# Optimization experiments

Measured on AMD Instinct MI355X. Metric: run time of the kernel, lower is better.

Reference implementation:

```python
import jax, jax.numpy as jnp
import numpy as np

B, S, H, A = 64, 4096, 256, 128


def entmax15(z):
    # exact entmax-1.5 along the last axis (Peters & Martins 2019)
    z = z / 2.0
    z = z - jnp.max(z, axis=-1, keepdims=True)
    zs = -jnp.sort(-z, axis=-1)                      # descending sort
    n = zs.shape[-1]
    k = jnp.arange(1, n + 1, dtype=z.dtype)
    mean = jnp.cumsum(zs, axis=-1) / k
    mean_sq = jnp.cumsum(zs * zs, axis=-1) / k
    ss = k * (mean_sq - mean * mean)
    delta = jnp.clip((1.0 - ss) / k, 0.0)
    tau = mean - jnp.sqrt(delta)
    k_star = jnp.sum(tau <= zs, axis=-1)             # support size per row
    tau_star = jnp.take_along_axis(tau, (k_star - 1)[..., None], axis=-1)
    return jnp.square(jnp.clip(z - tau_star, 0.0))


def setup_inputs() -> dict:
    key = jax.random.key(0)
    k0, k1, k2, k3, k4 = jax.random.split(key, 5)
    lim1 = 1.0 / np.sqrt(H)
    lim2 = 1.0 / np.sqrt(A)
    return {
        "lstm_output": jax.random.normal(k0, (B, S, H), dtype=jnp.float32),
        "W1": jax.random.uniform(k1, (H, A), jnp.float32, -lim1, lim1),
        "b1": jax.random.uniform(k2, (A,), jnp.float32, -lim1, lim1),
        "W2": jax.random.uniform(k3, (A, 1), jnp.float32, -lim2, lim2),
        "b2": jax.random.uniform(k4, (1,), jnp.float32, -lim2, lim2),
    }


def reference(lstm_output, W1, b1, W2, b2):
    # score MLP: Linear -> Tanh -> Linear -> squeeze(-1)  => [B, S]
    h = jnp.tanh(jnp.einsum("bsh,ha->bsa", lstm_output, W1) + b1)
    scores = (jnp.einsum("bsa,ao->bso", h, W2) + b2)[..., 0]
    weights = entmax15(scores)                       # entmax over seq axis (dim=1)
    context = jnp.einsum("bsh,bs->bh", lstm_output, weights)
    return (context, weights)
```

## Files before the change

### kernel.cpp

```cpp
#include <hip/hip_runtime.h>
#include <hip/hip_bf16.h>

#define BB 64
#define SS 4096
#define HH 256
#define AA 128
#define MT 128
#define BK 64
#define XST 72

typedef __fp16 fp16v2 __attribute__((ext_vector_type(2)));
typedef _Float16 half4v __attribute__((ext_vector_type(4)));
typedef _Float16 half8v __attribute__((ext_vector_type(8)));
typedef float floatx16 __attribute__((ext_vector_type(16)));

__device__ __forceinline__ float fast_tanh(float x) {
    float xc = fminf(fmaxf(x, -9.0f), 9.0f);
    float e = __expf(2.0f * xc);
    return 1.0f - __fdividef(2.0f, e + 1.0f);
}

__global__ void convert_w1(const float* __restrict__ W1, _Float16* __restrict__ Wt) {
    int n = blockIdx.x;
    int k = threadIdx.x;
    Wt[n * HH + k] = (_Float16)W1[k * AA + n];
}

__global__ __launch_bounds__(256) void score_mfma(
    const float* __restrict__ X,
    const _Float16* __restrict__ Wt,
    const float* __restrict__ b1,
    const float* __restrict__ W2,
    const float* __restrict__ b2,
    float* __restrict__ scores)
{
    __shared__ float smem_f[9216];
    _Float16* Xs = (_Float16*)smem_f;
    _Float16* Ws = (_Float16*)smem_f + MT * XST;
    float* part = smem_f;

    const int tid   = threadIdx.x;
    const int m0    = blockIdx.x * MT;
    const int wid   = tid >> 6;
    const int lane  = tid & 63;
    const int lrow  = lane & 31;
    const int lhalf = lane >> 5;
    const int wr    = (wid & 1) * 64;
    const int wc    = (wid >> 1) * 64;

    floatx16 acc[2][2];
    #pragma unroll
    for (int i = 0; i < 2; ++i)
        #pragma unroll
        for (int j = 0; j < 2; ++j)
            #pragma unroll
            for (int r = 0; r < 16; ++r) acc[i][j][r] = 0.0f;

    for (int k0 = 0; k0 < HH; k0 += BK) {
        #pragma unroll
        for (int p = 0; p < 8; ++p) {
            int idx = tid + p * 256;
            int row = idx >> 4, c4 = idx & 15;
            float4 v = *(const float4*)(X + (size_t)(m0 + row) * HH + k0 + c4 * 4);
            union { fp16v2 h2[2]; half4v h4; } u;
            u.h2[0] = __builtin_amdgcn_cvt_pkrtz(v.x, v.y);
            u.h2[1] = __builtin_amdgcn_cvt_pkrtz(v.z, v.w);
            *(half4v*)(Xs + row * XST + c4 * 4) = u.h4;
        }
        #pragma unroll
        for (int p = 0; p < 4; ++p) {
            int idx = tid + p * 256;
            int n = idx >> 3, u2 = idx & 7;
            *(uint4*)(Ws + n * XST + u2 * 8) =
                *(const uint4*)(Wt + (size_t)n * HH + k0 + u2 * 8);
        }
        __syncthreads();
        #pragma unroll
        for (int kk = 0; kk < BK; kk += 16) {
            half8v a0 = *(half8v*)(Xs + (wr + lrow) * XST + kk + lhalf * 8);
            half8v a1 = *(half8v*)(Xs + (wr + 32 + lrow) * XST + kk + lhalf * 8);
            half8v b0 = *(half8v*)(Ws + (wc + lrow) * XST + kk + lhalf * 8);
            half8v bq = *(half8v*)(Ws + (wc + 32 + lrow) * XST + kk + lhalf * 8);
            acc[0][0] = __builtin_amdgcn_mfma_f32_32x32x16_f16(a0, b0, acc[0][0], 0, 0, 0);
            acc[0][1] = __builtin_amdgcn_mfma_f32_32x32x16_f16(a0, bq, acc[0][1], 0, 0, 0);
            acc[1][0] = __builtin_amdgcn_mfma_f32_32x32x16_f16(a1, b0, acc[1][0], 0, 0, 0);
            acc[1][1] = __builtin_amdgcn_mfma_f32_32x32x16_f16(a1, bq, acc[1][1], 0, 0, 0);
        }
        __syncthreads();
    }

    const int cA = wc + lrow;
    const int cB = wc + 32 + lrow;
    const float b1A = b1[cA], b1B = b1[cB];
    const float w2A = W2[cA], w2B = W2[cB];
    #pragma unroll
    for (int i = 0; i < 2; ++i) {
        #pragma unroll
        for (int r = 0; r < 16; ++r) {
            float hA = fast_tanh(acc[i][0][r] + b1A) * w2A;
            float hB = fast_tanh(acc[i][1][r] + b1B) * w2B;
            int row = wr + i * 32 + (r & 3) + 8 * (r >> 2) + 4 * lhalf;
            part[row * 65 + (wid >> 1) * 32 + lrow] = hA + hB;
        }
    }
    __syncthreads();
    if (tid < MT) {
        float s = b2[0];
        #pragma unroll
        for (int c = 0; c < 64; ++c) s += part[tid * 65 + c];
        scores[m0 + tid] = s;
    }
}

__global__ __launch_bounds__(256) void entmax_ctx_kernel(
    const float* __restrict__ X, float* __restrict__ buf, float* __restrict__ ctx)
{
    __shared__ float sred[8];
    __shared__ int   cnt;
    __shared__ int   sidx[SS];
    __shared__ float swt[SS];

    const int b = blockIdx.x, tid = threadIdx.x;
    const int wid = tid >> 6;
    float* p = buf + (size_t)b * SS;
    const float4* p4 = (const float4*)p;

    if (tid == 0) cnt = 0;

    float z[16];
    #pragma unroll
    for (int jj = 0; jj < 4; ++jj) {
        float4 v = p4[tid * 4 + jj];
        z[jj * 4 + 0] = v.x * 0.5f; z[jj * 4 + 1] = v.y * 0.5f;
        z[jj * 4 + 2] = v.z * 0.5f; z[jj * 4 + 3] = v.w * 0.5f;
    }

    float m = -1e30f;
    #pragma unroll
    for (int j = 0; j < 16; ++j) m = fmaxf(m, z[j]);
    #pragma unroll
    for (int o = 1; o < 64; o <<= 1) m = fmaxf(m, __shfl_xor(m, o));
    if ((tid & 63) == 0) sred[wid] = m;
    __syncthreads();
    m = fmaxf(fmaxf(sred[0], sred[1]), fmaxf(sred[2], sred[3]));
    __syncthreads();
    #pragma unroll
    for (int j = 0; j < 16; ++j) z[j] -= m;

    float lo = -1.0f, hi = 0.0f;
    #pragma unroll 1
    for (int it = 0; it < 10; ++it) {
        float tau = 0.5f * (lo + hi);
        float s0 = 0.f, s1 = 0.f, s2 = 0.f, s3 = 0.f;
        #pragma unroll
        for (int j = 0; j < 16; j += 4) {
            float d0 = fmaxf(z[j]     - tau, 0.0f);
            float d1 = fmaxf(z[j + 1] - tau, 0.0f);
            float d2 = fmaxf(z[j + 2] - tau, 0.0f);
            float d3 = fmaxf(z[j + 3] - tau, 0.0f);
            s0 = fmaf(d0, d0, s0); s1 = fmaf(d1, d1, s1);
            s2 = fmaf(d2, d2, s2); s3 = fmaf(d3, d3, s3);
        }
        float s = (s0 + s1) + (s2 + s3);
        #pragma unroll
        for (int o = 1; o < 64; o <<= 1) s += __shfl_xor(s, o);
        if ((tid & 63) == 0) sred[wid] = s;
        __syncthreads();
        s = (sred[0] + sred[1]) + (sred[2] + sred[3]);
        __syncthreads();
        if (s >= 1.0f) lo = tau; else hi = tau;
    }

    float tau = lo;
    #pragma unroll 1
    for (int it = 0; it < 4; ++it) {
        float s0 = 0.f, s1 = 0.f, t0 = 0.f, t1 = 0.f;
        #pragma unroll
        for (int j = 0; j < 16; j += 2) {
            float d0 = fmaxf(z[j]     - tau, 0.0f);
            float d1 = fmaxf(z[j + 1] - tau, 0.0f);
            s0 = fmaf(d0, d0, s0); s1 = fmaf(d1, d1, s1);
            t0 += d0; t1 += d1;
        }
        float s = s0 + s1, t = t0 + t1;
        #pragma unroll
        for (int o = 1; o < 64; o <<= 1) {
            s += __shfl_xor(s, o);
            t += __shfl_xor(t, o);
        }
        if ((tid & 63) == 0) { sred[wid * 2] = s; sred[wid * 2 + 1] = t; }
        __syncthreads();
        s = (sred[0] + sred[2]) + (sred[4] + sred[6]);
        t = (sred[1] + sred[3]) + (sred[5] + sred[7]);
        __syncthreads();
        tau = fminf(tau + (s - 1.0f) / (2.0f * t + 1e-30f), hi);
    }

    float4* p4w = (float4*)p;
    #pragma unroll
    for (int jj = 0; jj < 4; ++jj) {
        float w[4];
        #pragma unroll
        for (int k = 0; k < 4; ++k) {
            float d = fmaxf(z[jj * 4 + k] - tau, 0.0f);
            w[k] = d * d;
            if (w[k] > 0.0f) {
                int pos = atomicAdd(&cnt, 1);
                sidx[pos] = tid * 16 + jj * 4 + k;
                swt[pos]  = w[k];
            }
        }
        p4w[tid * 4 + jj] = make_float4(w[0], w[1], w[2], w[3]);
    }
    __syncthreads();

    const int n = cnt;
    const float* xb = X + (size_t)b * SS * HH + tid;
    float a0 = 0.f, a1 = 0.f, a2 = 0.f, a3 = 0.f;
    int i = 0;
    for (; i + 4 <= n; i += 4) {
        a0 = fmaf(swt[i    ], xb[(size_t)sidx[i    ] * HH], a0);
        a1 = fmaf(swt[i + 1], xb[(size_t)sidx[i + 1] * HH], a1);
        a2 = fmaf(swt[i + 2], xb[(size_t)sidx[i + 2] * HH], a2);
        a3 = fmaf(swt[i + 3], xb[(size_t)sidx[i + 3] * HH], a3);
    }
    for (; i < n; ++i) a0 = fmaf(swt[i], xb[(size_t)sidx[i] * HH], a0);
    ctx[b * HH + tid] = (a0 + a1) + (a2 + a3);
}

extern "C" void kernel_launch(void* const* d_in, const int* in_sizes, int n_in,
                              void* d_out, int out_size, void* d_ws, size_t ws_size,
                              hipStream_t stream) {
    const float* X  = (const float*)d_in[0];
    const float* W1 = (const float*)d_in[1];
    const float* b1 = (const float*)d_in[2];
    const float* W2 = (const float*)d_in[3];
    const float* b2 = (const float*)d_in[4];

    float* out = (float*)d_out;
    float* ctx = out;
    float* wts = out + BB * HH;
    _Float16* Wt = (_Float16*)d_ws;

    convert_w1<<<AA, HH, 0, stream>>>(W1, Wt);
    score_mfma<<<(BB * SS) / MT, 256, 0, stream>>>(X, Wt, b1, W2, b2, wts);
    entmax_ctx_kernel<<<BB, 256, 0, stream>>>(X, wts, ctx);
}
```

Before: 391.2 us.

## Stream X directly from global into MFMA registers, keep whole W1 in LDS

The score kernel now loads the full fp16 W1 (128x256) into LDS once per block. Each wave owns 32 rows and reads its X operands straight from global memory into registers, prefetching one k-step ahead, instead of staging X through LDS with per-k-tile syncs. The tanh/W2 reduction is done with wave shuffles rather than a shared partial buffer, and launch bounds request 2 blocks per SM. This removes the LDS round trip and barriers for X, but raises per-block LDS use (~66KB), which may limit occupancy, and global loads of X are less coalesced (32-byte chunks per lane).

```diff
diff --git a/kernel.cpp b/kernel.cpp
--- a/kernel.cpp
+++ b/kernel.cpp
@@ -6,11 +6,9 @@
 #define HH 256
 #define AA 128
 #define MT 128
-#define BK 64
-#define XST 72
+#define WST 264
 
 typedef __fp16 fp16v2 __attribute__((ext_vector_type(2)));
-typedef _Float16 half4v __attribute__((ext_vector_type(4)));
 typedef _Float16 half8v __attribute__((ext_vector_type(8)));
 typedef float floatx16 __attribute__((ext_vector_type(16)));
 
@@ -26,7 +24,7 @@
     Wt[n * HH + k] = (_Float16)W1[k * AA + n];
 }
 
-__global__ __launch_bounds__(256) void score_mfma(
+__global__ __launch_bounds__(256, 2) void score_mfma(
     const float* __restrict__ X,
     const _Float16* __restrict__ Wt,
     const float* __restrict__ b1,
@@ -34,10 +32,7 @@
     const float* __restrict__ b2,
     float* __restrict__ scores)
 {
-    __shared__ float smem_f[9216];
-    _Float16* Xs = (_Float16*)smem_f;
-    _Float16* Ws = (_Float16*)smem_f + MT * XST;
-    float* part = smem_f;
+    __shared__ _Float16 Ws2[128 * WST];
 
     const int tid   = threadIdx.x;
     const int m0    = blockIdx.x * MT;
@@ -45,70 +40,65 @@
     const int lane  = tid & 63;
     const int lrow  = lane & 31;
     const int lhalf = lane >> 5;
-    const int wr    = (wid & 1) * 64;
-    const int wc    = (wid >> 1) * 64;
-
-    floatx16 acc[2][2];
-    #pragma unroll
-    for (int i = 0; i < 2; ++i)
-        #pragma unroll
-        for (int j = 0; j < 2; ++j)
-            #pragma unroll
-            for (int r = 0; r < 16; ++r) acc[i][j][r] = 0.0f;
-
-    for (int k0 = 0; k0 < HH; k0 += BK) {
-        #pragma unroll
-        for (int p = 0; p < 8; ++p) {
-            int idx = tid + p * 256;
-            int row = idx >> 4, c4 = idx & 15;
-            float4 v = *(const float4*)(X + (size_t)(m0 + row) * HH + k0 + c4 * 4);
-            union { fp16v2 h2[2]; half4v h4; } u;
-            u.h2[0] = __builtin_amdgcn_cvt_pkrtz(v.x, v.y);
-            u.h2[1] = __builtin_amdgcn_cvt_pkrtz(v.z, v.w);
-            *(half4v*)(Xs + row * XST + c4 * 4) = u.h4;
-        }
-        #pragma unroll
-        for (int p = 0; p < 4; ++p) {
-            int idx = tid + p * 256;
-            int n = idx >> 3, u2 = idx & 7;
-            *(uint4*)(Ws + n * XST + u2 * 8) =
-                *(const uint4*)(Wt + (size_t)n * HH + k0 + u2 * 8);
-        }
-        __syncthreads();
-        #pragma unroll
-        for (int kk = 0; kk < BK; kk += 16) {
-            half8v a0 = *(half8v*)(Xs + (wr + lrow) * XST + kk + lhalf * 8);
-            half8v a1 = *(half8v*)(Xs + (wr + 32 + lrow) * XST + kk + lhalf * 8);
-            half8v b0 = *(half8v*)(Ws + (wc + lrow) * XST + kk + lhalf * 8);
-            half8v bq = *(half8v*)(Ws + (wc + 32 + lrow) * XST + kk + lhalf * 8);
-            acc[0][0] = __builtin_amdgcn_mfma_f32_32x32x16_f16(a0, b0, acc[0][0], 0, 0, 0);
-            acc[0][1] = __builtin_amdgcn_mfma_f32_32x32x16_f16(a0, bq, acc[0][1], 0, 0, 0);
-            acc[1][0] = __builtin_amdgcn_mfma_f32_32x32x16_f16(a1, b0, acc[1][0], 0, 0, 0);
-            acc[1][1] = __builtin_amdgcn_mfma_f32_32x32x16_f16(a1, bq, acc[1][1], 0, 0, 0);
-        }
-        __syncthreads();
-    }
-
-    const int cA = wc + lrow;
-    const int cB = wc + 32 + lrow;
-    const float b1A = b1[cA], b1B = b1[cB];
-    const float w2A = W2[cA], w2B = W2[cB];
-    #pragma unroll
-    for (int i = 0; i < 2; ++i) {
-        #pragma unroll
-        for (int r = 0; r < 16; ++r) {
-            float hA = fast_tanh(acc[i][0][r] + b1A) * w2A;
-            float hB = fast_tanh(acc[i][1][r] + b1B) * w2B;
-            int row = wr + i * 32 + (r & 3) + 8 * (r >> 2) + 4 * lhalf;
-            part[row * 65 + (wid >> 1) * 32 + lrow] = hA + hB;
-        }
-    }
-    __syncthreads();
-    if (tid < MT) {
-        float s = b2[0];
-        #pragma unroll
-        for (int c = 0; c < 64; ++c) s += part[tid * 65 + c];
-        scores[m0 + tid] = s;
+
+    #pragma unroll
+    for (int p = 0; p < 16; ++p) {
+        int idx = tid + p * 256;
+        int row = idx >> 5, u = idx & 31;
+        *(uint4*)(Ws2 + row * WST + u * 8) =
+            *(const uint4*)(Wt + (size_t)row * HH + u * 8);
+    }
+    __syncthreads();
+
+    floatx16 acc[4];
+    #pragma unroll
+    for (int nb = 0; nb < 4; ++nb)
+        #pragma unroll
+        for (int r = 0; r < 16; ++r) acc[nb][r] = 0.0f;
+
+    const float* xrow = X + (size_t)(m0 + wid * 32 + lrow) * HH + lhalf * 8;
+
+    float4 a0 = *(const float4*)(xrow);
+    float4 a1 = *(const float4*)(xrow + 4);
+    #pragma unroll
+    for (int s = 0; s < 16; ++s) {
+        float4 n0 = a0, n1 = a1;
+        if (s < 15) {
+            n0 = *(const float4*)(xrow + (s + 1) * 16);
+            n1 = *(const float4*)(xrow + (s + 1) * 16 + 4);
+        }
+        union { fp16v2 h2[4]; half8v h8; } ua;
+        ua.h2[0] = __builtin_amdgcn_cvt_pkrtz(a0.x, a0.y);
+        ua.h2[1] = __builtin_amdgcn_cvt_pkrtz(a0.z, a0.w);
+        ua.h2[2] = __builtin_amdgcn_cvt_pkrtz(a1.x, a1.y);
+        ua.h2[3] = __builtin_amdgcn_cvt_pkrtz(a1.z, a1.w);
+        #pragma unroll
+        for (int nb = 0; nb < 4; ++nb) {
+            half8v bf = *(half8v*)(Ws2 + (nb * 32 + lrow) * WST + s * 16 + lhalf * 8);
+            acc[nb] = __builtin_amdgcn_mfma_f32_32x32x16_f16(ua.h8, bf, acc[nb], 0, 0, 0);
+        }
+        a0 = n0; a1 = n1;
+    }
+
+    const float b2v = b2[0];
+    float b1v[4], w2v[4];
+    #pragma unroll
+    for (int nb = 0; nb < 4; ++nb) {
+        b1v[nb] = b1[nb * 32 + lrow];
+        w2v[nb] = W2[nb * 32 + lrow];
+    }
+    #pragma unroll
+    for (int r = 0; r < 16; ++r) {
+        float s = 0.0f;
+        #pragma unroll
+        for (int nb = 0; nb < 4; ++nb)
+            s += fast_tanh(acc[nb][r] + b1v[nb]) * w2v[nb];
+        #pragma unroll
+        for (int o = 1; o < 32; o <<= 1) s += __shfl_xor(s, o);
+        if (lrow == 0) {
+            int ridx = (r & 3) + 8 * (r >> 2) + 4 * lhalf;
+            scores[m0 + wid * 32 + ridx] = s + b2v;
+        }
     }
 }
 
```

Result: slower. 406.7 us (+4.0%).
